# Optimization experiments

Measured on AMD Instinct MI355X. Metric: run time of the kernel, lower is better.

Reference implementation:

```python
import jax, jax.numpy as jnp
import numpy as np
from jax import lax

D_MODEL = 768
D_STATE = 64
BATCH = 2
SEQ = 2048


def setup_inputs() -> dict:
    key = jax.random.key(0)
    ks = jax.random.split(key, 12)
    d, n = D_MODEL, D_STATE
    x = jax.random.normal(ks[0], (BATCH, SEQ, d), dtype=jnp.float32)
    ln_gamma = jnp.ones((d,), jnp.float32)
    ln_beta = jnp.zeros((d,), jnp.float32)
    # nn.Linear default init ~ U(-1/sqrt(d), 1/sqrt(d))
    s = 1.0 / np.sqrt(d)
    W_in = jax.random.uniform(ks[1], (d, d), jnp.float32, -s, s)
    b_in = jax.random.uniform(ks[2], (d,), jnp.float32, -s, s)
    log_A = jax.random.normal(ks[3], (d, n), jnp.float32)
    B_p = jax.random.normal(ks[4], (d, n), jnp.float32) * 0.1
    C_p = jax.random.normal(ks[5], (d, n), jnp.float32) * 0.1
    D_p = jnp.ones((d,), jnp.float32)
    log_dt = jax.random.uniform(ks[6], (d,), jnp.float32) * 0.01 - 2.0
    W_out = jax.random.uniform(ks[7], (d, d), jnp.float32, -s, s)
    b_out = jax.random.uniform(ks[8], (d,), jnp.float32, -s, s)
    return {
        "x": x, "ln_gamma": ln_gamma, "ln_beta": ln_beta,
        "W_in": W_in, "b_in": b_in, "log_A": log_A,
        "B_p": B_p, "C_p": C_p, "D_p": D_p, "log_dt": log_dt,
        "W_out": W_out, "b_out": b_out,
    }


def reference(x, ln_gamma, ln_beta, W_in, b_in, log_A, B_p, C_p, D_p, log_dt, W_out, b_out):
    residual = x
    # LayerNorm (eps=1e-5, elementwise affine)
    mu = jnp.mean(x, axis=-1, keepdims=True)
    var = jnp.var(x, axis=-1, keepdims=True)
    xn = (x - mu) / jnp.sqrt(var + 1e-5) * ln_gamma + ln_beta
    # in_proj (torch Linear: x @ W^T + b)
    u = xn @ W_in.T + b_in  # [B,S,d]
    # Discretization
    A = -jnp.exp(log_A)                     # [d,N]
    dt = jnp.exp(log_dt)[:, None]           # [d,1]
    A_bar = jnp.exp(dt * A)                 # [d,N]
    B_bar = B_p * dt                        # [d,N]
    b, s, d = u.shape
    h0 = jnp.zeros((b, d, D_STATE), u.dtype)
    u_t = jnp.transpose(u, (1, 0, 2))       # [S,B,d]

    def step(h, xt):
        # h: [B,d,N], xt: [B,d]
        h = A_bar * h + B_bar * xt[:, :, None]
        y = jnp.einsum('bdn,dn->bd', h, C_p) + D_p * xt
        return h, y

    _, ys = lax.scan(step, h0, u_t)         # ys: [S,B,d]
    y = jnp.transpose(ys, (1, 0, 2))        # [B,S,d]
    y = y @ W_out.T + b_out
    # dropout is identity in eval mode
    return y + residual
```

## Files before the change

kernel.cpp:

```cpp
#include <hip/hip_runtime.h>
#include <math.h>

#define D_MODEL 768
#define D_STATE 64
#define BATCH   2
#define SEQ     2048
#define M_TOTAL (BATCH * SEQ)

typedef unsigned short ushort_t;
typedef float f32x4 __attribute__((ext_vector_type(4)));
typedef __bf16 bf16x8 __attribute__((ext_vector_type(8)));

__device__ __forceinline__ ushort_t f2bf(float f) {
    unsigned u = __float_as_uint(f);
    u = (u + 0x7FFFu + ((u >> 16) & 1u)) >> 16;
    return (ushort_t)u;
}

__device__ __forceinline__ void gload16(const void* g, void* shm) {
    __builtin_amdgcn_global_load_lds(
        (const __attribute__((address_space(1))) void*)g,
        (__attribute__((address_space(3))) void*)shm, 16, 0, 0);
}

__global__ __launch_bounds__(256) void pre_kernel(const float* __restrict__ x,
                                                  const float* __restrict__ gamma,
                                                  const float* __restrict__ beta,
                                                  ushort_t* __restrict__ xnb,
                                                  const float* __restrict__ W_in,
                                                  const float* __restrict__ W_out,
                                                  ushort_t* __restrict__ Winb,
                                                  ushort_t* __restrict__ Woutb) {
    int bx = blockIdx.x;
    if (bx >= 1024) {
        int b2 = bx - 1024;
        const float* src = (b2 < 576) ? W_in : W_out;
        ushort_t*    dst = (b2 < 576) ? Winb : Woutb;
        int blk = (b2 < 576) ? b2 : b2 - 576;
        int i = (blk * 256 + threadIdx.x) * 4;
        float4 v = *(const float4*)(src + i);
        ushort4 o = make_ushort4(f2bf(v.x), f2bf(v.y), f2bf(v.z), f2bf(v.w));
        *(ushort4*)(dst + i) = o;
        return;
    }
    int row  = bx * 4 + (threadIdx.x >> 6);
    int lane = threadIdx.x & 63;
    const float* xr = x + (size_t)row * D_MODEL;
    float4 v[3];
    v[0] = *(const float4*)(xr + lane * 4);
    v[1] = *(const float4*)(xr + 256 + lane * 4);
    v[2] = *(const float4*)(xr + 512 + lane * 4);
    float s = 0.f, ss = 0.f;
#pragma unroll
    for (int i = 0; i < 3; ++i) {
        s  += v[i].x + v[i].y + v[i].z + v[i].w;
        ss += v[i].x * v[i].x + v[i].y * v[i].y + v[i].z * v[i].z + v[i].w * v[i].w;
    }
#pragma unroll
    for (int off = 1; off < 64; off <<= 1) {
        s  += __shfl_xor(s, off, 64);
        ss += __shfl_xor(ss, off, 64);
    }
    float mean = s * (1.0f / 768.0f);
    float var  = ss * (1.0f / 768.0f) - mean * mean;
    float inv  = 1.0f / sqrtf(var + 1e-5f);
    ushort_t* xo = xnb + (size_t)row * D_MODEL;
#pragma unroll
    for (int i = 0; i < 3; ++i) {
        int c = i * 256 + lane * 4;
        float4 g  = *(const float4*)(gamma + c);
        float4 bb = *(const float4*)(beta + c);
        ushort4 o = make_ushort4(f2bf((v[i].x - mean) * inv * g.x + bb.x),
                                 f2bf((v[i].y - mean) * inv * g.y + bb.y),
                                 f2bf((v[i].z - mean) * inv * g.z + bb.z),
                                 f2bf((v[i].w - mean) * inv * g.w + bb.w));
        *(ushort4*)(xo + c) = o;
    }
}

#define ABUF  16384
#define BUFSZ 28672

__device__ __forceinline__ void gemm_core(const ushort_t* __restrict__ A,
                                          const ushort_t* __restrict__ B,
                                          const float* __restrict__ bias,
                                          char* smem, int tid, int bm, int bn,
                                          int w, int l, int wm, int wn,
                                          f32x4 acc[4][3], float biasv[3]) {
    int seg8 = ((l & 7) ^ (l >> 3)) * 8;
    const ushort_t* gA = A + (size_t)(bm + w * 32 + (l >> 3)) * D_MODEL + seg8;
    const ushort_t* gB = B + (size_t)(bn + w * 24 + (l >> 3)) * D_MODEL + seg8;
#pragma unroll
    for (int nt = 0; nt < 3; ++nt)
        biasv[nt] = bias[bn + wn + nt * 16 + (l & 15)];
#pragma unroll
    for (int q = 0; q < 4; ++q)
        gload16(gA + (size_t)(q * 8) * D_MODEL, smem + (w * 32 + q * 8) * 128);
#pragma unroll
    for (int q = 0; q < 3; ++q)
        gload16(gB + (size_t)(q * 8) * D_MODEL, smem + ABUF + (w * 24 + q * 8) * 128);
    __syncthreads();
    for (int it = 0; it < 12; ++it) {
        const char* cb = smem + (it & 1) * BUFSZ;
        if (it < 11) {
            char* nb = smem + ((it + 1) & 1) * BUFSZ;
            int k = (it + 1) * 64;
#pragma unroll
            for (int q = 0; q < 4; ++q)
                gload16(gA + (size_t)(q * 8) * D_MODEL + k, nb + (w * 32 + q * 8) * 128);
#pragma unroll
            for (int q = 0; q < 3; ++q)
                gload16(gB + (size_t)(q * 8) * D_MODEL + k, nb + ABUF + (w * 24 + q * 8) * 128);
        }
#pragma unroll
        for (int kk = 0; kk < 2; ++kk) {
            int sgb = kk * 4 + (l >> 4);
            bf16x8 af[4], bf[3];
#pragma unroll
            for (int mt = 0; mt < 4; ++mt) {
                int r = wm + mt * 16 + (l & 15);
                af[mt] = *(const bf16x8*)(cb + r * 128 + ((sgb ^ (r & 7)) * 16));
            }
#pragma unroll
            for (int nt = 0; nt < 3; ++nt) {
                int r = wn + nt * 16 + (l & 15);
                bf[nt] = *(const bf16x8*)(cb + ABUF + r * 128 + ((sgb ^ (r & 7)) * 16));
            }
#pragma unroll
            for (int mt = 0; mt < 4; ++mt)
#pragma unroll
                for (int nt = 0; nt < 3; ++nt)
                    acc[mt][nt] = __builtin_amdgcn_mfma_f32_16x16x32_bf16(af[mt], bf[nt], acc[mt][nt], 0, 0, 0);
        }
        __syncthreads();
    }
}

__global__ __launch_bounds__(256, 1) void gemm_in(const ushort_t* __restrict__ A,
                                                  const ushort_t* __restrict__ B,
                                                  const float* __restrict__ bias,
                                                  ushort_t* __restrict__ uTb) {
    __shared__ __align__(16) char smem[2 * BUFSZ];
    int tid = threadIdx.x;
    int w = tid >> 6, l = tid & 63;
    int bm = blockIdx.x * 128, bn = blockIdx.y * 96;
    int wm = (w & 1) * 64, wn = (w >> 1) * 48;
    f32x4 acc[4][3] = {};
    float biasv[3];
    gemm_core(A, B, bias, smem, tid, bm, bn, w, l, wm, wn, acc, biasv);

    ushort_t* T = (ushort_t*)smem;
#pragma unroll
    for (int mt = 0; mt < 4; ++mt)
#pragma unroll
        for (int nt = 0; nt < 3; ++nt)
#pragma unroll
            for (int i = 0; i < 4; ++i) {
                int n = wn + nt * 16 + (l & 15);
                int m = wm + mt * 16 + (l >> 4) * 4 + i;
                T[n * 136 + m] = f2bf(acc[mt][nt][i] + biasv[nt]);
            }
    __syncthreads();
    int b = bm >> 11, s0 = bm & 2047;
#pragma unroll
    for (int rep = 0; rep < 6; ++rep) {
        int idx = rep * 256 + tid;
        int row = idx >> 4, sg = idx & 15;
        uint4 v = *(const uint4*)&T[row * 136 + sg * 8];
        *(uint4*)(uTb + ((size_t)b * D_MODEL + bn + row) * SEQ + s0 + sg * 8) = v;
    }
}

__global__ __launch_bounds__(256, 1) void gemm_out(const ushort_t* __restrict__ A,
                                                   const ushort_t* __restrict__ B,
                                                   const float* __restrict__ bias,
                                                   const float* __restrict__ resid,
                                                   float* __restrict__ out) {
    __shared__ __align__(16) char smem[2 * BUFSZ];
    int tid = threadIdx.x;
    int w = tid >> 6, l = tid & 63;
    int bm = blockIdx.x * 128, bn = blockIdx.y * 96;
    int wm = (w & 1) * 64, wn = (w >> 1) * 48;
    f32x4 acc[4][3] = {};
    float biasv[3];
    gemm_core(A, B, bias, smem, tid, bm, bn, w, l, wm, wn, acc, biasv);

#pragma unroll
    for (int mt = 0; mt < 4; ++mt)
#pragma unroll
        for (int i = 0; i < 4; ++i) {
            int m = bm + wm + mt * 16 + (l >> 4) * 4 + i;
            const float* rp = resid + (size_t)m * D_MODEL + bn;
            float* op = out + (size_t)m * D_MODEL + bn;
#pragma unroll
            for (int nt = 0; nt < 3; ++nt) {
                int n = wn + nt * 16 + (l & 15);
                op[n] = acc[mt][nt][i] + biasv[nt] + rp[n];
            }
        }
}

#define OFF_U  0
#define OFF_V  9216
#define OFF_T  18432
#define OFF_M  27648
#define OFF_H  36864
#define OFF_W  46080
#define OFF_SM 63488

__global__ __launch_bounds__(256) void scan_mm(const ushort_t* __restrict__ uTb,
                                               const float* __restrict__ log_A,
                                               const float* __restrict__ B_p,
                                               const float* __restrict__ C_p,
                                               const float* __restrict__ D_p,
                                               const float* __restrict__ log_dt,
                                               ushort_t* __restrict__ yTb) {
    __shared__ __align__(16) char smem[65024];
    ushort_t* Up = (ushort_t*)(smem + OFF_U);
    ushort_t* Vp = (ushort_t*)(smem + OFF_V);
    ushort_t* Tp = (ushort_t*)(smem + OFF_T);
    ushort_t* Mp = (ushort_t*)(smem + OFF_M);
    ushort_t* Hp = (ushort_t*)(smem + OFF_H);
    float*    Wp = (float*)(smem + OFF_W);
    float*    Kp = (float*)(smem + OFF_W);
    float*    aArr  = (float*)(smem + OFF_SM);
    float*    BbArr = aArr + 64;
    float*    CcArr = aArr + 128;
    float*    CBArr = aArr + 192;
    float*    Kc    = aArr + 256;

    int d   = blockIdx.x;
    int tid = threadIdx.x;
    int w   = tid >> 6, l = tid & 63;

    if (tid < 64) {
        int n = tid;
        float dt = __expf(log_dt[d]);
        float a  = -dt * __expf(log_A[d * 64 + n]);
        float Bb = B_p[d * 64 + n] * dt;
        float Cc = C_p[d * 64 + n];
        aArr[n] = a; BbArr[n] = Bb; CcArr[n] = Cc; CBArr[n] = Cc * Bb;
    }
    __syncthreads();

    {
        int tau = tid & 63, part = tid >> 6;
        float s = 0.f;
#pragma unroll
        for (int i = 0; i < 16; ++i) {
            int n = part * 16 + i;
            s += CBArr[n] * __expf((float)tau * aArr[n]);
        }
        Kp[part * 64 + tau] = s;
    }
    __syncthreads();
    if (tid < 64)
        Kc[tid] = Kp[tid] + Kp[64 + tid] + Kp[128 + tid] + Kp[192 + tid]
                + (tid == 0 ? D_p[d] : 0.f);
    __syncthreads();

    {
        int r = tid >> 2, seg = (tid & 3) * 16;
        float a = aArr[r], Bb = BbArr[r];
#pragma unroll
        for (int i = 0; i < 16; ++i) {
            int s = seg + i;
            Vp[r * 72 + s] = f2bf(Bb * __expf((float)(63 - s) * a));
        }
#pragma unroll
        for (int i = 0; i < 16; ++i) {
            int n = seg + i;
            Mp[r * 72 + n] = f2bf(CcArr[n] * __expf((float)(r + 1) * aArr[n]));
        }
#pragma unroll
        for (int i = 0; i < 16; ++i) {
            int s = seg + i;
            Tp[r * 72 + s] = (s <= r) ? f2bf(Kc[r - s]) : (ushort_t)0;
        }
        int col = r, bu = col >> 5, cu = col & 31;
        const ushort_t* usrc = uTb + ((size_t)bu * D_MODEL + d) * SEQ + cu * 64 + seg;
        *(uint4*)(Up + col * 72 + seg)     = *(const uint4*)(usrc);
        *(uint4*)(Up + col * 72 + seg + 8) = *(const uint4*)(usrc + 8);
    }
    __syncthreads();

    {
        int p0 = w * 16;
        f32x4 acc1[4] = {};
#pragma unroll
        for (int kk = 0; kk < 2; ++kk) {
            int koff = kk * 32 + (l >> 4) * 8;
            bf16x8 af = *(const bf16x8*)(Vp + (p0 + (l & 15)) * 72 + koff);
#pragma unroll
            for (int qt = 0; qt < 4; ++qt) {
                bf16x8 bf = *(const bf16x8*)(Up + (qt * 16 + (l & 15)) * 72 + koff);
                acc1[qt] = __builtin_amdgcn_mfma_f32_16x16x32_bf16(af, bf, acc1[qt], 0, 0, 0);
            }
        }
#pragma unroll
        for (int qt = 0; qt < 4; ++qt)
#pragma unroll
            for (int i = 0; i < 4; ++i)
                Wp[(qt * 16 + (l & 15)) * 68 + p0 + (l >> 4) * 4 + i] = acc1[qt][i];
    }
    __syncthreads();

    if (tid < 128) {
        int b2 = tid >> 6, n = tid & 63;
        float Ab64 = __expf(64.f * aArr[n]);
        float H = 0.f;
#pragma unroll
        for (int c = 0; c < 32; ++c) {
            int col = b2 * 32 + c;
            Hp[col * 72 + n] = f2bf(H);
            H = fmaf(Ab64, H, Wp[col * 68 + n]);
        }
    }
    __syncthreads();

    {
        int j0 = w * 16;
        f32x4 accY[4] = {};
#pragma unroll
        for (int kk = 0; kk < 2; ++kk) {
            int koff = kk * 32 + (l >> 4) * 8;
            bf16x8 at = *(const bf16x8*)(Tp + (j0 + (l & 15)) * 72 + koff);
            bf16x8 am = *(const bf16x8*)(Mp + (j0 + (l & 15)) * 72 + koff);
#pragma unroll
            for (int qt = 0; qt < 4; ++qt) {
                bf16x8 bu = *(const bf16x8*)(Up + (qt * 16 + (l & 15)) * 72 + koff);
                bf16x8 bh = *(const bf16x8*)(Hp + (qt * 16 + (l & 15)) * 72 + koff);
                accY[qt] = __builtin_amdgcn_mfma_f32_16x16x32_bf16(at, bu, accY[qt], 0, 0, 0);
                accY[qt] = __builtin_amdgcn_mfma_f32_16x16x32_bf16(am, bh, accY[qt], 0, 0, 0);
            }
        }
#pragma unroll
        for (int qt = 0; qt < 4; ++qt)
#pragma unroll
            for (int i = 0; i < 4; ++i)
                Wp[(qt * 16 + (l & 15)) * 68 + j0 + (l >> 4) * 4 + i] = accY[qt][i];
    }
    __syncthreads();

    {
        int col = tid >> 2, jseg = (tid & 3) * 16;
        int b3 = col >> 5, c3 = col & 31;
        ushort_t* dst = yTb + ((size_t)b3 * D_MODEL + d) * SEQ + c3 * 64 + jseg;
#pragma unroll
        for (int q = 0; q < 4; ++q) {
            float4 v = *(const float4*)(Wp + col * 68 + jseg + q * 4);
            ushort4 o = make_ushort4(f2bf(v.x), f2bf(v.y), f2bf(v.z), f2bf(v.w));
            *(ushort4*)(dst + q * 4) = o;
        }
    }
}

__global__ __launch_bounds__(256) void tcast_kernel(const ushort_t* __restrict__ yTb,
                                                    ushort_t* __restrict__ yA) {
    __shared__ ushort_t T3[64 * 72];
    int t = threadIdx.x;
    int s0 = blockIdx.x * 64, d0 = blockIdx.y * 64, b = blockIdx.z;
    int dl = t >> 2, sq = (t & 3) * 16;
    const ushort_t* src = yTb + ((size_t)b * D_MODEL + d0 + dl) * SEQ + s0 + sq;
    ushort_t tmp[16];
    *(uint4*)tmp       = *(const uint4*)src;
    *(uint4*)(tmp + 8) = *(const uint4*)(src + 8);
#pragma unroll
    for (int i = 0; i < 16; ++i)
        T3[(sq + i) * 72 + dl] = tmp[i];
    __syncthreads();
    int sl = t >> 2, dseg = (t & 3) * 16;
    ushort_t* dst = yA + ((size_t)b * SEQ + s0 + sl) * D_MODEL + d0 + dseg;
    *(uint4*)dst       = *(const uint4*)&T3[sl * 72 + dseg];
    *(uint4*)(dst + 8) = *(const uint4*)&T3[sl * 72 + dseg + 8];
}

extern "C" void kernel_launch(void* const* d_in, const int* in_sizes, int n_in,
                              void* d_out, int out_size, void* d_ws, size_t ws_size,
                              hipStream_t stream) {
    const float* x        = (const float*)d_in[0];
    const float* ln_gamma = (const float*)d_in[1];
    const float* ln_beta  = (const float*)d_in[2];
    const float* W_in     = (const float*)d_in[3];
    const float* b_in     = (const float*)d_in[4];
    const float* log_A    = (const float*)d_in[5];
    const float* B_p      = (const float*)d_in[6];
    const float* C_p      = (const float*)d_in[7];
    const float* D_p      = (const float*)d_in[8];
    const float* log_dt   = (const float*)d_in[9];
    const float* W_out    = (const float*)d_in[10];
    const float* b_out    = (const float*)d_in[11];
    float* out = (float*)d_out;

    char* ws = (char*)d_ws;
    ushort_t* uTb   = (ushort_t*)(ws + 0);
    ushort_t* yTb   = (ushort_t*)(ws + 6291456);
    ushort_t* xnb   = (ushort_t*)(ws + 12582912);
    ushort_t* yA    = xnb;
    ushort_t* Winb  = (ushort_t*)(ws + 18874368);
    ushort_t* Woutb = (ushort_t*)(ws + 20054016);

    pre_kernel<<<dim3(1024 + 1152), 256, 0, stream>>>(x, ln_gamma, ln_beta, xnb,
                                                      W_in, W_out, Winb, Woutb);
    gemm_in<<<dim3(M_TOTAL / 128, D_MODEL / 96), 256, 0, stream>>>(xnb, Winb, b_in, uTb);
    scan_mm<<<dim3(D_MODEL), 256, 0, stream>>>(uTb, log_A, B_p, C_p, D_p, log_dt, yTb);
    tcast_kernel<<<dim3(SEQ / 64, D_MODEL / 64, BATCH), 256, 0, stream>>>(yTb, yA);
    gemm_out<<<dim3(M_TOTAL / 128, D_MODEL / 96), 256, 0, stream>>>(yA, Woutb, b_out, x, out);
}
```

Before: 129.8 us.

## Load GEMM fragments directly from global memory, drop LDS staging

Both GEMMs stop staging A/B tiles through LDS with global_load_lds double buffering and instead load MFMA fragments straight from global memory into registers, using a two-stage register double buffer. The in-projection epilogue writes the transposed bf16 output directly from accumulators instead of going through an LDS transpose. Launch bounds now allow two blocks per SM. This removes LDS traffic and barriers but relies on L1/L2 for reuse across waves, and its global reads and transposed stores are less coalesced.

```diff
diff --git a/kernel.cpp b/kernel.cpp
--- a/kernel.cpp
+++ b/kernel.cpp
@@ -15,12 +15,6 @@
     unsigned u = __float_as_uint(f);
     u = (u + 0x7FFFu + ((u >> 16) & 1u)) >> 16;
     return (ushort_t)u;
-}
-
-__device__ __forceinline__ void gload16(const void* g, void* shm) {
-    __builtin_amdgcn_global_load_lds(
-        (const __attribute__((address_space(1))) void*)g,
-        (__attribute__((address_space(3))) void*)shm, 16, 0, 0);
 }
 
 __global__ __launch_bounds__(256) void pre_kernel(const float* __restrict__ x,
@@ -78,113 +72,98 @@
     }
 }
 
-#define ABUF  16384
-#define BUFSZ 28672
+
+__device__ __forceinline__ void frag_load(const ushort_t* const pa[4],
+                                          const ushort_t* const pb[3],
+                                          int k, bf16x8 fa[4], bf16x8 fb[3]) {
+#pragma unroll
+    for (int mt = 0; mt < 4; ++mt) fa[mt] = *(const bf16x8*)(pa[mt] + k);
+#pragma unroll
+    for (int nt = 0; nt < 3; ++nt) fb[nt] = *(const bf16x8*)(pb[nt] + k);
+}
+
+__device__ __forceinline__ void frag_mma(const bf16x8 fa[4], const bf16x8 fb[3],
+                                         f32x4 acc[4][3]) {
+#pragma unroll
+    for (int mt = 0; mt < 4; ++mt)
+#pragma unroll
+        for (int nt = 0; nt < 3; ++nt)
+            acc[mt][nt] = __builtin_amdgcn_mfma_f32_16x16x32_bf16(fa[mt], fb[nt], acc[mt][nt], 0, 0, 0);
+}
 
 __device__ __forceinline__ void gemm_core(const ushort_t* __restrict__ A,
                                           const ushort_t* __restrict__ B,
-                                          const float* __restrict__ bias,
-                                          char* smem, int tid, int bm, int bn,
-                                          int w, int l, int wm, int wn,
-                                          f32x4 acc[4][3], float biasv[3]) {
-    int seg8 = ((l & 7) ^ (l >> 3)) * 8;
-    const ushort_t* gA = A + (size_t)(bm + w * 32 + (l >> 3)) * D_MODEL + seg8;
-    const ushort_t* gB = B + (size_t)(bn + w * 24 + (l >> 3)) * D_MODEL + seg8;
+                                          int bm, int bn, int wm, int wn, int l,
+                                          f32x4 acc[4][3]) {
+    int lr = l & 15, kq = (l >> 4) * 8;
+    const ushort_t* pa[4];
+    const ushort_t* pb[3];
+#pragma unroll
+    for (int mt = 0; mt < 4; ++mt)
+        pa[mt] = A + (size_t)(bm + wm + mt * 16 + lr) * D_MODEL + kq;
 #pragma unroll
     for (int nt = 0; nt < 3; ++nt)
-        biasv[nt] = bias[bn + wn + nt * 16 + (l & 15)];
-#pragma unroll
-    for (int q = 0; q < 4; ++q)
-        gload16(gA + (size_t)(q * 8) * D_MODEL, smem + (w * 32 + q * 8) * 128);
-#pragma unroll
-    for (int q = 0; q < 3; ++q)
-        gload16(gB + (size_t)(q * 8) * D_MODEL, smem + ABUF + (w * 24 + q * 8) * 128);
-    __syncthreads();
-    for (int it = 0; it < 12; ++it) {
-        const char* cb = smem + (it & 1) * BUFSZ;
-        if (it < 11) {
-            char* nb = smem + ((it + 1) & 1) * BUFSZ;
-            int k = (it + 1) * 64;
-#pragma unroll
-            for (int q = 0; q < 4; ++q)
-                gload16(gA + (size_t)(q * 8) * D_MODEL + k, nb + (w * 32 + q * 8) * 128);
-#pragma unroll
-            for (int q = 0; q < 3; ++q)
-                gload16(gB + (size_t)(q * 8) * D_MODEL + k, nb + ABUF + (w * 24 + q * 8) * 128);
-        }
-#pragma unroll
-        for (int kk = 0; kk < 2; ++kk) {
-            int sgb = kk * 4 + (l >> 4);
-            bf16x8 af[4], bf[3];
-#pragma unroll
-            for (int mt = 0; mt < 4; ++mt) {
-                int r = wm + mt * 16 + (l & 15);
-                af[mt] = *(const bf16x8*)(cb + r * 128 + ((sgb ^ (r & 7)) * 16));
-            }
-#pragma unroll
-            for (int nt = 0; nt < 3; ++nt) {
-                int r = wn + nt * 16 + (l & 15);
-                bf[nt] = *(const bf16x8*)(cb + ABUF + r * 128 + ((sgb ^ (r & 7)) * 16));
-            }
-#pragma unroll
-            for (int mt = 0; mt < 4; ++mt)
-#pragma unroll
-                for (int nt = 0; nt < 3; ++nt)
-                    acc[mt][nt] = __builtin_amdgcn_mfma_f32_16x16x32_bf16(af[mt], bf[nt], acc[mt][nt], 0, 0, 0);
-        }
-        __syncthreads();
-    }
-}
-
-__global__ __launch_bounds__(256, 1) void gemm_in(const ushort_t* __restrict__ A,
+        pb[nt] = B + (size_t)(bn + wn + nt * 16 + lr) * D_MODEL + kq;
+
+    bf16x8 fa0[4], fb0[3], fa1[4], fb1[3];
+    frag_load(pa, pb, 0, fa0, fb0);
+    for (int p = 0; p < 11; ++p) {
+        int k = p * 64;
+        frag_load(pa, pb, k + 32, fa1, fb1);
+        frag_mma(fa0, fb0, acc);
+        frag_load(pa, pb, k + 64, fa0, fb0);
+        frag_mma(fa1, fb1, acc);
+    }
+    frag_load(pa, pb, 736, fa1, fb1);
+    frag_mma(fa0, fb0, acc);
+    frag_mma(fa1, fb1, acc);
+}
+
+__global__ __launch_bounds__(256, 2) void gemm_in(const ushort_t* __restrict__ A,
                                                   const ushort_t* __restrict__ B,
                                                   const float* __restrict__ bias,
                                                   ushort_t* __restrict__ uTb) {
-    __shared__ __align__(16) char smem[2 * BUFSZ];
     int tid = threadIdx.x;
     int w = tid >> 6, l = tid & 63;
     int bm = blockIdx.x * 128, bn = blockIdx.y * 96;
     int wm = (w & 1) * 64, wn = (w >> 1) * 48;
     f32x4 acc[4][3] = {};
-    float biasv[3];
-    gemm_core(A, B, bias, smem, tid, bm, bn, w, l, wm, wn, acc, biasv);
-
-    ushort_t* T = (ushort_t*)smem;
-#pragma unroll
-    for (int mt = 0; mt < 4; ++mt)
-#pragma unroll
-        for (int nt = 0; nt < 3; ++nt)
-#pragma unroll
-            for (int i = 0; i < 4; ++i) {
-                int n = wn + nt * 16 + (l & 15);
-                int m = wm + mt * 16 + (l >> 4) * 4 + i;
-                T[n * 136 + m] = f2bf(acc[mt][nt][i] + biasv[nt]);
-            }
-    __syncthreads();
-    int b = bm >> 11, s0 = bm & 2047;
-#pragma unroll
-    for (int rep = 0; rep < 6; ++rep) {
-        int idx = rep * 256 + tid;
-        int row = idx >> 4, sg = idx & 15;
-        uint4 v = *(const uint4*)&T[row * 136 + sg * 8];
-        *(uint4*)(uTb + ((size_t)b * D_MODEL + bn + row) * SEQ + s0 + sg * 8) = v;
-    }
-}
-
-__global__ __launch_bounds__(256, 1) void gemm_out(const ushort_t* __restrict__ A,
+    gemm_core(A, B, bm, bn, wm, wn, l, acc);
+
+    int b = bm >> 11;
+    int sbase = (bm & 2047) + wm + (l >> 4) * 4;
+#pragma unroll
+    for (int nt = 0; nt < 3; ++nt) {
+        int n = bn + wn + nt * 16 + (l & 15);
+        float bv = bias[n];
+        ushort_t* rowp = uTb + ((size_t)b * D_MODEL + n) * SEQ;
+#pragma unroll
+        for (int mt = 0; mt < 4; ++mt) {
+            ushort4 o = make_ushort4(f2bf(acc[mt][nt][0] + bv),
+                                     f2bf(acc[mt][nt][1] + bv),
+                                     f2bf(acc[mt][nt][2] + bv),
+                                     f2bf(acc[mt][nt][3] + bv));
+            *(ushort4*)(rowp + sbase + mt * 16) = o;
+        }
+    }
+}
+
+__global__ __launch_bounds__(256, 2) void gemm_out(const ushort_t* __restrict__ A,
                                                    const ushort_t* __restrict__ B,
                                                    const float* __restrict__ bias,
                                                    const float* __restrict__ resid,
                                                    float* __restrict__ out) {
-    __shared__ __align__(16) char smem[2 * BUFSZ];
     int tid = threadIdx.x;
     int w = tid >> 6, l = tid & 63;
     int bm = blockIdx.x * 128, bn = blockIdx.y * 96;
     int wm = (w & 1) * 64, wn = (w >> 1) * 48;
     f32x4 acc[4][3] = {};
+    gemm_core(A, B, bm, bn, wm, wn, l, acc);
+
     float biasv[3];
-    gemm_core(A, B, bias, smem, tid, bm, bn, w, l, wm, wn, acc, biasv);
-
+#pragma unroll
+    for (int nt = 0; nt < 3; ++nt)
+        biasv[nt] = bias[bn + wn + nt * 16 + (l & 15)];
 #pragma unroll
     for (int mt = 0; mt < 4; ++mt)
 #pragma unroll
```

After: 158.3 us. 22.0% more time.
